# Optimization experiments

Hardware: AMD Instinct MI355X
Metric: run time of the kernel (lower is better)

The kernel has to match this reference:

```python
import jax, jax.numpy as jnp
import numpy as np

B = 131072
EPS = 1e-5

def _attn(x, Wq, Wk, Wv, Wo):
    # x: (B, 10, 1); Wq/Wk/Wv: (1, 16); Wo: (16, 1)
    Q = x @ Wq  # (B, 10, 16)
    K = x @ Wk
    V = x @ Wv
    A = jnp.einsum('bqd,bkd->bqk', Q, K) / 4.0  # sqrt(16) = 4
    A = jax.nn.softmax(A, axis=1)  # NOTE: torch Softmax(dim=1) -> axis 1, not -1
    out = jnp.einsum('bqk,bkd->bqd', A, V) @ Wo  # (B, 10, 1)
    return out[..., 0]  # squeeze -> (B, 10)

def _bn(h, gamma, beta):
    # BatchNorm1d training-mode math (batch stats, biased variance)
    mu = jnp.mean(h, axis=0)
    var = jnp.mean(jnp.square(h - mu), axis=0)
    return gamma * (h - mu) * jax.lax.rsqrt(var + EPS) + beta

def setup_inputs() -> dict:
    key = jax.random.key(0)
    ks = jax.random.split(key, 24)
    n = lambda k, shp, s=1.0: (jax.random.normal(k, shp, dtype=jnp.float32) * s)
    inp = {
        'x':   n(ks[0], (B, 10, 1)),
        'Wq1': n(ks[1], (1, 16)), 'Wk1': n(ks[2], (1, 16)),
        'Wv1': n(ks[3], (1, 16)), 'Wo1': n(ks[4], (16, 1)),
        'Wq2': n(ks[5], (1, 16)), 'Wk2': n(ks[6], (1, 16)),
        'Wv2': n(ks[7], (1, 16)), 'Wo2': n(ks[8], (16, 1)),
        # layer1: Linear(10,128) BN ReLU Linear(128,256) BN ReLU Linear(256,10)
        'W1a': n(ks[9], (10, 128), 0.3), 'b1a': jnp.zeros((128,), jnp.float32),
        'g1a': jnp.ones((128,), jnp.float32), 'be1a': jnp.zeros((128,), jnp.float32),
        'W1b': n(ks[10], (128, 256), 0.09), 'b1b': jnp.zeros((256,), jnp.float32),
        'g1b': jnp.ones((256,), jnp.float32), 'be1b': jnp.zeros((256,), jnp.float32),
        'W1c': n(ks[11], (256, 10), 0.06), 'b1c': jnp.zeros((10,), jnp.float32),
        # layer2: Linear(10,128) BN ReLU Linear(128,256) BN ReLU Linear(256,2)
        'W2a': n(ks[12], (10, 128), 0.3), 'b2a': jnp.zeros((128,), jnp.float32),
        'g2a': jnp.ones((128,), jnp.float32), 'be2a': jnp.zeros((128,), jnp.float32),
        'W2b': n(ks[13], (128, 256), 0.09), 'b2b': jnp.zeros((256,), jnp.float32),
        'g2b': jnp.ones((256,), jnp.float32), 'be2b': jnp.zeros((256,), jnp.float32),
        'W2c': n(ks[14], (256, 2), 0.06), 'b2c': jnp.zeros((2,), jnp.float32),
    }
    return inp

def reference(x, Wq1, Wk1, Wv1, Wo1, Wq2, Wk2, Wv2, Wo2,
              W1a, b1a, g1a, be1a, W1b, b1b, g1b, be1b, W1c, b1c,
              W2a, b2a, g2a, be2a, W2b, b2b, g2b, be2b, W2c, b2c):
    h = _attn(x, Wq1, Wk1, Wv1, Wo1)                 # (B, 10)
    h = jax.nn.relu(_bn(h @ W1a + b1a, g1a, be1a))   # (B, 128)
    h = jax.nn.relu(_bn(h @ W1b + b1b, g1b, be1b))   # (B, 256)
    h = h @ W1c + b1c                                # (B, 10)
    h = _attn(h[..., None], Wq2, Wk2, Wv2, Wo2)      # (B, 10)
    h = jax.nn.relu(_bn(h @ W2a + b2a, g2a, be2a))   # (B, 128)
    h = jax.nn.relu(_bn(h @ W2b + b2b, g2b, be2b))   # (B, 256)
    return h @ W2c + b2c                             # (B, 2)
```

## Files before the change

kernel.cpp:

```cpp
#include <hip/hip_runtime.h>
#include <hip/hip_bf16.h>

#define EPS 1e-5f
constexpr int BN = 131072;
constexpr int NBKT = 32;
constexpr int NTILE = BN/64;
constexpr int TILE_ELEMS = 256*64;

typedef __attribute__((ext_vector_type(8))) short bf16x8;
typedef __attribute__((ext_vector_type(4))) float f32x4;

constexpr size_t OFF_H   = 0;
constexpr size_t OFF_HH  = OFF_H  + (size_t)BN*10;
constexpr size_t OFF_M1  = OFF_HH + (size_t)BN*10;
constexpr size_t OFF_S2  = OFF_M1 + 65;
constexpr size_t OFF_M3  = OFF_S2 + 512;
constexpr size_t OFF_S4  = OFF_M3 + 65;
constexpr size_t OFF_WA1 = OFF_S4 + 512;
constexpr size_t OFF_BA1 = OFF_WA1 + 1280;
constexpr size_t OFF_WA2 = OFF_BA1 + 128;
constexpr size_t OFF_BA2 = OFF_WA2 + 1280;
constexpr size_t OFF_SC2 = OFF_BA2 + 128;
constexpr size_t OFF_TC2 = OFF_SC2 + 256;
constexpr size_t OFF_SC4 = OFF_TC2 + 256;
constexpr size_t OFF_TC4 = OFF_SC4 + 256;
constexpr size_t OFF_WB1 = OFF_TC4 + 256;
constexpr size_t OFF_BB1 = OFF_WB1 + 32768;
constexpr size_t OFF_WB2 = OFF_BB1 + 256;
constexpr size_t OFF_BB2 = OFF_WB2 + 32768;
constexpr size_t OFF_P1  = OFF_BB2 + 256;
constexpr size_t OFF_P3  = OFF_P1 + 1024*65;
constexpr size_t OFF_S2B = OFF_P3 + 1024*65;
constexpr size_t OFF_S4B = OFF_S2B + (size_t)NBKT*512;
constexpr size_t OFF_WT1 = OFF_S4B + (size_t)NBKT*512;
constexpr size_t OFF_WT2 = OFF_WT1 + 16384;
constexpr size_t OFF_END = OFF_WT2 + 16384;
constexpr size_t OFF_Z_BYTES = ((OFF_END*4 + 255) & ~(size_t)255);
constexpr size_t WS_NEED = OFF_Z_BYTES + (size_t)NTILE*TILE_ELEMS*2;

__device__ __forceinline__ float wsum(float v){
  v += __shfl_down(v, 32);
  v += __shfl_down(v, 16);
  v += __shfl_down(v, 8);
  v += __shfl_down(v, 4);
  v += __shfl_down(v, 2);
  v += __shfl_down(v, 1);
  return v;
}

__device__ __forceinline__ unsigned pk_bf16(float a, float b){
  union { __hip_bfloat16 h[2]; unsigned u; } cv;
  cv.h[0] = __float2bfloat16(a);
  cv.h[1] = __float2bfloat16(b);
  return cv.u;
}

__device__ __forceinline__ unsigned short bf16_1(float a){
  union { __hip_bfloat16 h; unsigned short u; } cv;
  cv.h = __float2bfloat16(a);
  return cv.u;
}

__device__ __forceinline__ float bf16_to_f(unsigned short u){
  return __uint_as_float(((unsigned)u) << 16);
}

__device__ __forceinline__ void attn10(const float* xr, float cqk, float cvo, float* y){
  #pragma unroll
  for (int q=0;q<10;q++) y[q] = 0.f;
  #pragma unroll
  for (int k=0;k<10;k++){
    float t = cqk * xr[k];
    float m = t*xr[0];
    #pragma unroll
    for (int q=1;q<10;q++) m = fmaxf(m, t*xr[q]);
    float ex[10]; float s = 0.f;
    #pragma unroll
    for (int q=0;q<10;q++){ ex[q] = __expf(t*xr[q]-m); s += ex[q]; }
    float f = xr[k]/s;
    #pragma unroll
    for (int q=0;q<10;q++) y[q] += ex[q]*f;
  }
  #pragma unroll
  for (int q=0;q<10;q++) y[q] *= cvo;
}

__device__ __forceinline__ void moments_block(const float* y, float (*red)[65],
                                              float* Pb, int t){
  int lane = t & 63, w = t >> 6;
  #pragma unroll
  for (int i=0;i<10;i++){
    float v = wsum(y[i]);
    if (lane==0) red[w][i] = v;
  }
  #pragma unroll
  for (int i=0;i<10;i++){
    #pragma unroll
    for (int j=i;j<10;j++){
      float v = wsum(y[i]*y[j]);
      if (lane==0) red[w][10 + 10*i - i*(i-1)/2 + (j-i)] = v;
    }
  }
  __syncthreads();
  if (t < 65)
    Pb[(size_t)blockIdx.x*65 + t] = red[0][t]+red[1][t]+red[2][t]+red[3][t];
}

__device__ __forceinline__ void moments10(const float* y, float* M, int lane){
  #pragma unroll
  for (int i=0;i<10;i++){
    float s = wsum(y[i]);
    if (lane==0) atomicAdd(&M[i], s);
  }
  #pragma unroll
  for (int i=0;i<10;i++){
    #pragma unroll
    for (int j=i;j<10;j++){
      int id = 10*i - i*(i-1)/2 + (j-i);
      float s = wsum(y[i]*y[j]);
      if (lane==0) atomicAdd(&M[10+id], s);
    }
  }
}

__global__ __launch_bounds__(256) void k_attn_in(
    const float* __restrict__ x,
    const float* __restrict__ Wq, const float* __restrict__ Wk,
    const float* __restrict__ Wv, const float* __restrict__ Wo,
    float* __restrict__ h, float* __restrict__ Pb){
  __shared__ float xs[256][11];
  __shared__ float red[4][65];
  int t = threadIdx.x;
  size_t base = (size_t)blockIdx.x*2560;
  for (int idx=t; idx<2560; idx+=256) xs[idx/10][idx%10] = x[base+idx];
  float cqk=0.f, cvo=0.f;
  #pragma unroll
  for (int d=0;d<16;d++){ cqk += Wq[d]*Wk[d]; cvo += Wv[d]*Wo[d]; }
  cqk *= 0.25f;
  __syncthreads();
  float xr[10];
  #pragma unroll
  for (int q=0;q<10;q++) xr[q] = xs[t][q];
  float y[10];
  attn10(xr, cqk, cvo, y);
  #pragma unroll
  for (int q=0;q<10;q++) xs[t][q] = y[q];
  moments_block(y, red, Pb, t);
  for (int idx=t; idx<2560; idx+=256) h[base+idx] = xs[idx/10][idx%10];
}

__global__ void k_fold10_part(const float* __restrict__ Pb, int npart,
                              const float* __restrict__ W,
                              const float* __restrict__ bv, const float* __restrict__ g,
                              const float* __restrict__ be,
                              float* __restrict__ WT, float* __restrict__ bo){
  __shared__ float part[65][8];
  __shared__ float sM[65];
  int t = threadIdx.x;
  if (t < 520){
    int c = t>>3, k = t&7;
    int n = npart>>3;
    float acc = 0.f;
    #pragma unroll 4
    for (int i=0;i<n;i++) acc += Pb[(size_t)(k*n+i)*65 + c];
    part[c][k] = acc;
  }
  __syncthreads();
  if (t < 65){
    float a = 0.f;
    #pragma unroll
    for (int k=0;k<8;k++) a += part[t][k];
    sM[t] = a;
  }
  __syncthreads();
  int j = t;
  if (j >= 128) return;
  const float invB = 1.f/(float)BN;
  float Eh[10];
  #pragma unroll
  for (int i=0;i<10;i++) Eh[i] = sM[i]*invB;
  float wj[10];
  #pragma unroll
  for (int i=0;i<10;i++) wj[i] = W[i*128+j];
  float mu = bv[j];
  #pragma unroll
  for (int i=0;i<10;i++) mu += Eh[i]*wj[i];
  float var = 0.f;
  #pragma unroll
  for (int i=0;i<10;i++){
    #pragma unroll
    for (int l=0;l<10;l++){
      int a = i<l ? i : l, c = i<l ? l : i;
      int id = 10*a - a*(a-1)/2 + (c-a);
      float cov = sM[10+id]*invB - Eh[i]*Eh[l];
      var += wj[i]*wj[l]*cov;
    }
  }
  float s = g[j]*rsqrtf(var + EPS);
  #pragma unroll
  for (int i=0;i<10;i++) WT[j*10+i] = wj[i]*s;
  bo[j] = (bv[j]-mu)*s + be[j];
}

__global__ void k_fold10_atomic(const float* __restrict__ M,
                                const float* __restrict__ W,
                                const float* __restrict__ bv, const float* __restrict__ g,
                                const float* __restrict__ be,
                                float* __restrict__ WT, float* __restrict__ bo){
  int j = threadIdx.x;
  if (j >= 128) return;
  const float invB = 1.f/(float)BN;
  float Eh[10];
  #pragma unroll
  for (int i=0;i<10;i++) Eh[i] = M[i]*invB;
  float wj[10];
  #pragma unroll
  for (int i=0;i<10;i++) wj[i] = W[i*128+j];
  float mu = bv[j];
  #pragma unroll
  for (int i=0;i<10;i++) mu += Eh[i]*wj[i];
  float var = 0.f;
  #pragma unroll
  for (int i=0;i<10;i++){
    #pragma unroll
    for (int l=0;l<10;l++){
      int a = i<l ? i : l, c = i<l ? l : i;
      int id = 10*a - a*(a-1)/2 + (c-a);
      float cov = M[10+id]*invB - Eh[i]*Eh[l];
      var += wj[i]*wj[l]*cov;
    }
  }
  float s = g[j]*rsqrtf(var + EPS);
  #pragma unroll
  for (int i=0;i<10;i++) WT[j*10+i] = wj[i]*s;
  bo[j] = (bv[j]-mu)*s + be[j];
}

__global__ void k_fold_affine(const float* __restrict__ stats,
                              const float* __restrict__ g,
                              const float* __restrict__ be,
                              float* __restrict__ s, float* __restrict__ tt){
  int j = threadIdx.x;
  if (j >= 256) return;
  float su = 0.f, sq = 0.f;
  #pragma unroll 4
  for (int k=0;k<NBKT;k++){
    su += stats[k*512 + j];
    sq += stats[k*512 + 256 + j];
  }
  const float invB = 1.f/(float)BN;
  float mu  = su*invB;
  float var = sq*invB - mu*mu;
  float sc = g[j]*rsqrtf(var + EPS);
  s[j]  = sc;
  tt[j] = be[j] - mu*sc;
}

__global__ __launch_bounds__(256) void k_prep_wt2(
    const float* __restrict__ W1, const float* __restrict__ W2,
    unsigned short* __restrict__ WT1, unsigned short* __restrict__ WT2){
  int g = blockIdx.x;
  const float* W = (g < 128) ? W1 : W2;
  unsigned short* WT = (g < 128) ? WT1 : WT2;
  int idx = (g & 127)*256 + threadIdx.x;
  int c = idx >> 7, k = idx & 127;
  WT[idx] = bf16_1(W[k*256 + c]);
}

__device__ __forceinline__ void block_gemm(
    const float* __restrict__ h, const float* __restrict__ WaT,
    const float* __restrict__ ba, const unsigned short* __restrict__ WT,
    unsigned short* h1s, float (*hs)[11], float* sWaT,
    f32x4 (&acc)[4][4], int t, size_t row0)
{
  int lane = t & 63, w = t >> 6;
  int ci = lane & 15, g = lane >> 4;

  bf16x8 bfr[4][4];
  #pragma unroll
  for (int nt=0; nt<4; nt++)
    #pragma unroll
    for (int kt=0; kt<4; kt++){
      union { uint4 u; bf16x8 v; } cv;
      cv.u = *(const uint4*)(WT + (size_t)(w*64 + nt*16 + ci)*128 + kt*32 + g*8);
      bfr[nt][kt] = cv.v;
    }

  for (int idx = t; idx < 640; idx += 256) hs[idx/10][idx%10] = h[row0*10 + idx];
  for (int idx = t; idx < 1280; idx += 256) sWaT[idx] = WaT[idx];
  __syncthreads();

  {
    int r = lane;
    int i0 = w * 32;
    float hr[10];
    #pragma unroll
    for (int l=0;l<10;l++) hr[l] = hs[r][l];
    #pragma unroll
    for (int j=0;j<4;j++){
      unsigned pk[4];
      #pragma unroll
      for (int q=0;q<4;q++){
        int i = i0 + j*8 + q*2;
        float v0 = ba[i], v1 = ba[i+1];
        #pragma unroll
        for (int l=0;l<10;l++){
          v0 = fmaf(hr[l], sWaT[i*10+l],     v0);
          v1 = fmaf(hr[l], sWaT[(i+1)*10+l], v1);
        }
        pk[q] = pk_bf16(fmaxf(v0,0.f), fmaxf(v1,0.f));
      }
      int byte = r*256 + (((i0 + j*8)*2) ^ ((r&7)<<4));
      *(uint4*)((char*)h1s + byte) = make_uint4(pk[0],pk[1],pk[2],pk[3]);
    }
  }
  __syncthreads();

  #pragma unroll
  for (int mt=0;mt<4;mt++)
    #pragma unroll
    for (int nt=0;nt<4;nt++)
      acc[mt][nt] = (f32x4){0.f,0.f,0.f,0.f};

  #pragma unroll
  for (int mt=0; mt<4; mt++){
    int r = mt*16 + ci;
    bf16x8 af[4];
    #pragma unroll
    for (int kt=0; kt<4; kt++){
      int byte = r*256 + ((kt*64 + g*16) ^ ((r&7)<<4));
      af[kt] = *(const bf16x8*)((const char*)h1s + byte);
    }
    #pragma unroll
    for (int nt=0; nt<4; nt++)
      #pragma unroll
      for (int kt=0; kt<4; kt++)
        acc[mt][nt] = __builtin_amdgcn_mfma_f32_16x16x32_bf16(
            af[kt], bfr[nt][kt], acc[mt][nt], 0, 0, 0);
  }
}

__global__ __launch_bounds__(256) void k_layer_mfma(
    const float* __restrict__ h,
    const float* __restrict__ WaT,
    const float* __restrict__ ba,
    const unsigned short* __restrict__ WT,
    const float* __restrict__ bb,
    unsigned short* __restrict__ zt,
    float* __restrict__ stats)
{
  __shared__ __align__(16) char smem[36864];
  unsigned short* h1s = (unsigned short*)smem;
  float (*hs)[11]     = (float(*)[11])(smem + 16384);
  float* sWaT         = (float*)(smem + 19200);
  unsigned short* zs  = (unsigned short*)smem;
  int t = threadIdx.x;
  int lane = t & 63, w = t >> 6;
  int ci = lane & 15, g = lane >> 4;
  size_t row0 = (size_t)blockIdx.x * 64;

  f32x4 acc[4][4];
  block_gemm(h, WaT, ba, WT, h1s, hs, sWaT, acc, t, row0);

  float bbv[4];
  #pragma unroll
  for (int nt=0;nt<4;nt++) bbv[nt] = bb[w*64 + nt*16 + ci];
  float s1v[4], s2v[4];
  #pragma unroll
  for (int nt=0; nt<4; nt++){
    float cs = 0.f, cq = 0.f;
    #pragma unroll
    for (int mt=0; mt<4; mt++)
      #pragma unroll
      for (int j=0;j<4;j++){
        float zv = acc[mt][nt][j] + bbv[nt];
        acc[mt][nt][j] = zv;
        cs += zv;
        cq += zv*zv;
      }
    cs += __shfl_down(cs, 32); cs += __shfl_down(cs, 16);
    cq += __shfl_down(cq, 32); cq += __shfl_down(cq, 16);
    s1v[nt] = cs; s2v[nt] = cq;
  }
  __syncthreads();

  #pragma unroll
  for (int mt=0; mt<4; mt++)
    #pragma unroll
    for (int nt=0; nt<4; nt++){
      int c = w*64 + nt*16 + ci;
      int r0 = mt*16 + g*4;
      uint2 v;
      v.x = pk_bf16(acc[mt][nt][0], acc[mt][nt][1]);
      v.y = pk_bf16(acc[mt][nt][2], acc[mt][nt][3]);
      *(uint2*)&zs[c*72 + r0] = v;
    }
  __syncthreads();

  size_t tbase = (size_t)blockIdx.x * TILE_ELEMS;
  #pragma unroll
  for (int pass=0; pass<8; pass++){
    int c  = (t>>3) + pass*32;
    int rc = (t&7)*8;
    uint4 v = *(const uint4*)&zs[c*72 + rc];
    *(uint4*)(zt + tbase + c*64 + rc) = v;
  }

  if (lane < 16){
    int bkt = blockIdx.x & (NBKT-1);
    #pragma unroll
    for (int nt=0; nt<4; nt++){
      int c = w*64 + nt*16 + ci;
      atomicAdd(&stats[bkt*512 + c],       s1v[nt]);
      atomicAdd(&stats[bkt*512 + 256 + c], s2v[nt]);
    }
  }
}

__global__ __launch_bounds__(256) void k_consume_mid(
    const unsigned short* __restrict__ zt,
    const float* __restrict__ s_g, const float* __restrict__ t_g,
    const float* __restrict__ Wc,  const float* __restrict__ bc,
    const float* __restrict__ Wq, const float* __restrict__ Wk,
    const float* __restrict__ Wv, const float* __restrict__ Wo,
    float* __restrict__ hh, float* __restrict__ Pb){
  __shared__ __align__(16) unsigned short zs[2][32*256];
  __shared__ __align__(16) float sWc[256*12];
  __shared__ float ss[256], st[256];
  __shared__ float red[4][65];
  int t = threadIdx.x;
  for (int idx=t; idx<2560; idx+=256) sWc[(idx/10)*12 + (idx%10)] = Wc[idx];
  ss[t] = s_g[t]; st[t] = t_g[t];
  size_t b0 = (size_t)blockIdx.x*256;

  float z3[10];
  #pragma unroll
  for (int l=0;l<10;l++) z3[l] = bc[l];

  int q = t >> 6, l = t & 63;
  size_t src_base = ((size_t)blockIdx.x*4 + q)*TILE_ELEMS + l*32;
  int dst_off = (l>>1)*256 + q*64 + (l&1)*32;
  uint4 r0, r1, r2, r3;
  {
    const uint4* src = (const uint4*)(zt + src_base);
    r0 = src[0]; r1 = src[1]; r2 = src[2]; r3 = src[3];
    uint4* dst = (uint4*)&zs[0][dst_off];
    dst[0] = r0; dst[1] = r1; dst[2] = r2; dst[3] = r3;
  }
  for (int cc=0; cc<8; cc++){
    __syncthreads();
    if (cc < 7){
      const uint4* src = (const uint4*)(zt + src_base + (size_t)(cc+1)*2048);
      r0 = src[0]; r1 = src[1]; r2 = src[2]; r3 = src[3];
    }
    const unsigned short* zb = zs[cc&1];
    #pragma unroll 4
    for (int cl=0; cl<32; cl++){
      int c = cc*32 + cl;
      float f = bf16_to_f(zb[cl*256 + t]);
      float h2 = fmaxf(fmaf(ss[c], f, st[c]), 0.f);
      const float4* wr = (const float4*)&sWc[c*12];
      float4 w0 = wr[0];
      float4 w1 = wr[1];
      float2 w2 = *(const float2*)&sWc[c*12 + 8];
      z3[0] = fmaf(h2, w0.x, z3[0]); z3[1] = fmaf(h2, w0.y, z3[1]);
      z3[2] = fmaf(h2, w0.z, z3[2]); z3[3] = fmaf(h2, w0.w, z3[3]);
      z3[4] = fmaf(h2, w1.x, z3[4]); z3[5] = fmaf(h2, w1.y, z3[5]);
      z3[6] = fmaf(h2, w1.z, z3[6]); z3[7] = fmaf(h2, w1.w, z3[7]);
      z3[8] = fmaf(h2, w2.x, z3[8]); z3[9] = fmaf(h2, w2.y, z3[9]);
    }
    if (cc < 7){
      uint4* dst = (uint4*)&zs[(cc+1)&1][dst_off];
      dst[0] = r0; dst[1] = r1; dst[2] = r2; dst[3] = r3;
    }
  }

  float cqk=0.f, cvo=0.f;
  #pragma unroll
  for (int d=0;d<16;d++){ cqk += Wq[d]*Wk[d]; cvo += Wv[d]*Wo[d]; }
  cqk *= 0.25f;
  float y[10];
  attn10(z3, cqk, cvo, y);
  __syncthreads();
  float* hhs = (float*)zs[0];
  #pragma unroll
  for (int qq=0;qq<10;qq++) hhs[t*10+qq] = y[qq];
  moments_block(y, red, Pb, t);
  for (int idx=t; idx<2560; idx+=256)
    hh[b0*10 + idx] = hhs[idx];
}

__global__ __launch_bounds__(256) void k_consume_out(
    const unsigned short* __restrict__ zt,
    const float* __restrict__ s_g, const float* __restrict__ t_g,
    const float* __restrict__ Wc,  const float* __restrict__ bc,
    float* __restrict__ out){
  __shared__ __align__(16) unsigned short zs[2][32*256];
  __shared__ __align__(8) float sWo[512];
  __shared__ float ss[256], st[256];
  int t = threadIdx.x;
  sWo[t] = Wc[t]; sWo[256+t] = Wc[256+t];
  ss[t] = s_g[t]; st[t] = t_g[t];
  size_t b0 = (size_t)blockIdx.x*256;
  float o0 = bc[0], o1 = bc[1];
  int q = t >> 6, l = t & 63;
  size_t src_base = ((size_t)blockIdx.x*4 + q)*TILE_ELEMS + l*32;
  int dst_off = (l>>1)*256 + q*64 + (l&1)*32;
  uint4 r0, r1, r2, r3;
  {
    const uint4* src = (const uint4*)(zt + src_base);
    r0 = src[0]; r1 = src[1]; r2 = src[2]; r3 = src[3];
    uint4* dst = (uint4*)&zs[0][dst_off];
    dst[0] = r0; dst[1] = r1; dst[2] = r2; dst[3] = r3;
  }
  for (int cc=0; cc<8; cc++){
    __syncthreads();
    if (cc < 7){
      const uint4* src = (const uint4*)(zt + src_base + (size_t)(cc+1)*2048);
      r0 = src[0]; r1 = src[1]; r2 = src[2]; r3 = src[3];
    }
    const unsigned short* zb = zs[cc&1];
    #pragma unroll 8
    for (int cl=0; cl<32; cl++){
      int c = cc*32 + cl;
      float f = bf16_to_f(zb[cl*256 + t]);
      float h5 = fmaxf(fmaf(ss[c], f, st[c]), 0.f);
      float2 wv = *(const float2*)&sWo[c*2];
      o0 = fmaf(h5, wv.x, o0);
      o1 = fmaf(h5, wv.y, o1);
    }
    if (cc < 7){
      uint4* dst = (uint4*)&zs[(cc+1)&1][dst_off];
      dst[0] = r0; dst[1] = r1; dst[2] = r2; dst[3] = r3;
    }
  }
  *(float2*)(out + (b0 + t)*2) = make_float2(o0, o1);
}

__global__ void k_fold_big(const float* __restrict__ stats,
                           const float* __restrict__ W,
                           const float* __restrict__ bv, const float* __restrict__ g,
                           const float* __restrict__ be,
                           float* __restrict__ Wf, float* __restrict__ bf){
  int j = blockIdx.x*256 + threadIdx.x;
  if (j >= 256) return;
  const float invB = 1.f/(float)BN;
  float mu  = stats[j]*invB;
  float var = stats[256+j]*invB - mu*mu;
  float s = g[j]*rsqrtf(var + EPS);
  bf[j] = (bv[j]-mu)*s + be[j];
  for (int i=0;i<128;i++) Wf[i*256+j] = W[i*256+j]*s;
}

__global__ __launch_bounds__(256) void k_mid(
    const float* __restrict__ h,
    const float* __restrict__ WaT, const float* __restrict__ ba,
    const float* __restrict__ Wb,  const float* __restrict__ bb,
    float* __restrict__ stats){
  int b = blockIdx.x*256 + threadIdx.x;
  if (b >= BN) return;
  float hr[10];
  #pragma unroll
  for (int l=0;l<10;l++) hr[l] = h[(size_t)b*10+l];
  int lane = threadIdx.x & 63;
  for (int jc=0;jc<4;jc++){
    float acc[64];
    #pragma unroll
    for (int j=0;j<64;j++) acc[j] = bb[jc*64+j];
    for (int i=0;i<128;i++){
      float h1 = ba[i];
      #pragma unroll
      for (int l=0;l<10;l++) h1 += hr[l]*WaT[i*10+l];
      h1 = fmaxf(h1, 0.f);
      const float* __restrict__ w = &Wb[i*256 + jc*64];
      #pragma unroll
      for (int j=0;j<64;j++) acc[j] += h1*w[j];
    }
    #pragma unroll
    for (int j=0;j<64;j++){
      float s1 = wsum(acc[j]);
      float s2 = wsum(acc[j]*acc[j]);
      if (lane==0){
        atomicAdd(&stats[jc*64+j], s1);
        atomicAdd(&stats[256+jc*64+j], s2);
      }
    }
  }
}

__global__ __launch_bounds__(256) void k_mid2(
    const float* __restrict__ h,
    const float* __restrict__ WaT, const float* __restrict__ ba,
    const float* __restrict__ Wbf, const float* __restrict__ bbf,
    const float* __restrict__ Wc,  const float* __restrict__ bc,
    const float* __restrict__ Wq, const float* __restrict__ Wk,
    const float* __restrict__ Wv, const float* __restrict__ Wo,
    float* __restrict__ hh, float* __restrict__ M){
  int b = blockIdx.x*256 + threadIdx.x;
  if (b >= BN) return;
  float hr[10];
  #pragma unroll
  for (int l=0;l<10;l++) hr[l] = h[(size_t)b*10+l];
  float z3[10];
  #pragma unroll
  for (int l=0;l<10;l++) z3[l] = bc[l];
  for (int jc=0;jc<4;jc++){
    float acc[64];
    #pragma unroll
    for (int j=0;j<64;j++) acc[j] = bbf[jc*64+j];
    for (int i=0;i<128;i++){
      float h1 = ba[i];
      #pragma unroll
      for (int l=0;l<10;l++) h1 += hr[l]*WaT[i*10+l];
      h1 = fmaxf(h1, 0.f);
      const float* __restrict__ w = &Wbf[i*256 + jc*64];
      #pragma unroll
      for (int j=0;j<64;j++) acc[j] += h1*w[j];
    }
    #pragma unroll
    for (int j=0;j<64;j++){
      float h2 = fmaxf(acc[j], 0.f);
      const float* __restrict__ wc = &Wc[(jc*64+j)*10];
      #pragma unroll
      for (int l=0;l<10;l++) z3[l] += h2*wc[l];
    }
  }
  float cqk=0.f, cvo=0.f;
  #pragma unroll
  for (int d=0;d<16;d++){ cqk += Wq[d]*Wk[d]; cvo += Wv[d]*Wo[d]; }
  cqk *= 0.25f;
  float y[10];
  attn10(z3, cqk, cvo, y);
  #pragma unroll
  for (int q=0;q<10;q++) hh[(size_t)b*10+q] = y[q];
  moments10(y, M, threadIdx.x & 63);
}

__global__ __launch_bounds__(256) void k_out(
    const float* __restrict__ h,
    const float* __restrict__ WaT, const float* __restrict__ ba,
    const float* __restrict__ Wbf, const float* __restrict__ bbf,
    const float* __restrict__ Wc,  const float* __restrict__ bc,
    float* __restrict__ out){
  int b = blockIdx.x*256 + threadIdx.x;
  if (b >= BN) return;
  float hr[10];
  #pragma unroll
  for (int l=0;l<10;l++) hr[l] = h[(size_t)b*10+l];
  float o0 = bc[0], o1 = bc[1];
  for (int jc=0;jc<4;jc++){
    float acc[64];
    #pragma unroll
    for (int j=0;j<64;j++) acc[j] = bbf[jc*64+j];
    for (int i=0;i<128;i++){
      float h4 = ba[i];
      #pragma unroll
      for (int l=0;l<10;l++) h4 += hr[l]*WaT[i*10+l];
      h4 = fmaxf(h4, 0.f);
      const float* __restrict__ w = &Wbf[i*256 + jc*64];
      #pragma unroll
      for (int j=0;j<64;j++) acc[j] += h4*w[j];
    }
    #pragma unroll
    for (int j=0;j<64;j++){
      float h5 = fmaxf(acc[j], 0.f);
      o0 += h5*Wc[(jc*64+j)*2];
      o1 += h5*Wc[(jc*64+j)*2+1];
    }
  }
  out[(size_t)b*2]   = o0;
  out[(size_t)b*2+1] = o1;
}

extern "C" void kernel_launch(void* const* d_in, const int* in_sizes, int n_in,
                              void* d_out, int out_size, void* d_ws, size_t ws_size,
                              hipStream_t stream){
  const float* x   = (const float*)d_in[0];
  const float* Wq1 = (const float*)d_in[1];
  const float* Wk1 = (const float*)d_in[2];
  const float* Wv1 = (const float*)d_in[3];
  const float* Wo1 = (const float*)d_in[4];
  const float* Wq2 = (const float*)d_in[5];
  const float* Wk2 = (const float*)d_in[6];
  const float* Wv2 = (const float*)d_in[7];
  const float* Wo2 = (const float*)d_in[8];
  const float* W1a = (const float*)d_in[9];  const float* b1a = (const float*)d_in[10];
  const float* g1a = (const float*)d_in[11]; const float* be1a= (const float*)d_in[12];
  const float* W1b = (const float*)d_in[13]; const float* b1b = (const float*)d_in[14];
  const float* g1b = (const float*)d_in[15]; const float* be1b= (const float*)d_in[16];
  const float* W1c = (const float*)d_in[17]; const float* b1c = (const float*)d_in[18];
  const float* W2a = (const float*)d_in[19]; const float* b2a = (const float*)d_in[20];
  const float* g2a = (const float*)d_in[21]; const float* be2a= (const float*)d_in[22];
  const float* W2b = (const float*)d_in[23]; const float* b2b = (const float*)d_in[24];
  const float* g2b = (const float*)d_in[25]; const float* be2b= (const float*)d_in[26];
  const float* W2c = (const float*)d_in[27]; const float* b2c = (const float*)d_in[28];

  float* f   = (float*)d_ws;
  float* h   = f + OFF_H;
  float* hh  = f + OFF_HH;
  float* M1  = f + OFF_M1;
  float* S2  = f + OFF_S2;
  float* M3  = f + OFF_M3;
  float* S4  = f + OFF_S4;
  float* WA1 = f + OFF_WA1; float* BA1 = f + OFF_BA1;
  float* WA2 = f + OFF_WA2; float* BA2 = f + OFF_BA2;
  float* SC2 = f + OFF_SC2; float* TC2 = f + OFF_TC2;
  float* SC4 = f + OFF_SC4; float* TC4 = f + OFF_TC4;
  float* WB1 = f + OFF_WB1; float* BB1 = f + OFF_BB1;
  float* WB2 = f + OFF_WB2; float* BB2 = f + OFF_BB2;
  float* P1  = f + OFF_P1;  float* P3  = f + OFF_P3;
  float* S2B = f + OFF_S2B; float* S4B = f + OFF_S4B;
  unsigned short* WT1 = (unsigned short*)(f + OFF_WT1);
  unsigned short* WT2 = (unsigned short*)(f + OFF_WT2);
  unsigned short* ZT = (unsigned short*)((char*)d_ws + OFF_Z_BYTES);

  dim3 blk(256);
  dim3 grid256(BN/256);
  dim3 grid64(BN/64);

  if (ws_size >= WS_NEED){
    hipMemsetAsync(S2B, 0, (size_t)2*NBKT*512*sizeof(float), stream);
    k_prep_wt2<<<256,blk,0,stream>>>(W1b, W2b, WT1, WT2);
    k_attn_in<<<grid256,blk,0,stream>>>(x, Wq1,Wk1,Wv1,Wo1, h, P1);
    k_fold10_part<<<1,576,0,stream>>>(P1, 512, W1a,b1a,g1a,be1a, WA1,BA1);
    k_layer_mfma<<<grid64,blk,0,stream>>>(h, WA1,BA1, WT1,b1b, ZT, S2B);
    k_fold_affine<<<1,256,0,stream>>>(S2B, g1b, be1b, SC2, TC2);
    k_consume_mid<<<grid256,blk,0,stream>>>(ZT, SC2,TC2, W1c,b1c,
                                            Wq2,Wk2,Wv2,Wo2, hh, P3);
    k_fold10_part<<<1,576,0,stream>>>(P3, 512, W2a,b2a,g2a,be2a, WA2,BA2);
    k_layer_mfma<<<grid64,blk,0,stream>>>(hh, WA2,BA2, WT2,b2b, ZT, S4B);
    k_fold_affine<<<1,256,0,stream>>>(S4B, g2b, be2b, SC4, TC4);
    k_consume_out<<<grid256,blk,0,stream>>>(ZT, SC4,TC4, W2c,b2c, (float*)d_out);
  } else {
    hipMemsetAsync(M1, 0, (65+512+65+512)*sizeof(float), stream);
    k_attn_in<<<grid256,blk,0,stream>>>(x, Wq1,Wk1,Wv1,Wo1, h, P1);
    k_fold10_part<<<1,576,0,stream>>>(P1, 512, W1a,b1a,g1a,be1a, WA1,BA1);
    k_mid<<<grid256,blk,0,stream>>>(h, WA1,BA1, W1b,b1b, S2);
    k_fold_big<<<1,256,0,stream>>>(S2, W1b,b1b,g1b,be1b, WB1,BB1);
    k_mid2<<<grid256,blk,0,stream>>>(h, WA1,BA1, WB1,BB1, W1c,b1c,
                                     Wq2,Wk2,Wv2,Wo2, hh, M3);
    k_fold10_atomic<<<1,128,0,stream>>>(M3, W2a,b2a,g2a,be2a, WA2,BA2);
    k_mid<<<grid256,blk,0,stream>>>(hh, WA2,BA2, W2b,b2b, S4);
    k_fold_big<<<1,256,0,stream>>>(S4, W2b,b2b,g2b,be2b, WB2,BB2);
    k_out<<<grid256,blk,0,stream>>>(hh, WA2,BA2, WB2,BB2, W2c,b2c, (float*)d_out);
  }
}
```

Baseline: 214.9 us.

## Process two 64-row tiles per block and store GEMM output directly

k_layer_mfma now handles 128 rows per block as two 64-row tiles. The bf16 weight fragments held in registers are reused across both tiles, halving their global loads and the number of atomic stat flushes per row. The LDS transpose staging of the output is dropped: each lane writes its packed 8-byte values straight to the tiled global buffer, and the second tile's layer-a compute goes into a separate LDS buffer. The direct stores are narrower and less coalesced than the old 16-byte ones, and halving the grid reduces block-level parallelism.

```diff
diff --git a/kernel.cpp b/kernel.cpp
--- a/kernel.cpp
+++ b/kernel.cpp
@@ -267,14 +267,22 @@
   WT[idx] = bf16_1(W[k*256 + c]);
 }
 
-__device__ __forceinline__ void block_gemm(
-    const float* __restrict__ h, const float* __restrict__ WaT,
-    const float* __restrict__ ba, const unsigned short* __restrict__ WT,
-    unsigned short* h1s, float (*hs)[11], float* sWaT,
-    f32x4 (&acc)[4][4], int t, size_t row0)
+__global__ __launch_bounds__(256) void k_layer_mfma(
+    const float* __restrict__ h,
+    const float* __restrict__ WaT,
+    const float* __restrict__ ba,
+    const unsigned short* __restrict__ WT,
+    const float* __restrict__ bb,
+    unsigned short* __restrict__ zt,
+    float* __restrict__ stats)
 {
+  __shared__ unsigned short h1s[2][64*128];
+  __shared__ float hs[128][11];
+  __shared__ float sWaT[1280];
+  int t = threadIdx.x;
   int lane = t & 63, w = t >> 6;
   int ci = lane & 15, g = lane >> 4;
+  size_t row0 = (size_t)blockIdx.x * 128;
 
   bf16x8 bfr[4][4];
   #pragma unroll
@@ -286,9 +294,14 @@
       bfr[nt][kt] = cv.v;
     }
 
-  for (int idx = t; idx < 640; idx += 256) hs[idx/10][idx%10] = h[row0*10 + idx];
+  for (int idx = t; idx < 1280; idx += 256) hs[idx/10][idx%10] = h[row0*10 + idx];
   for (int idx = t; idx < 1280; idx += 256) sWaT[idx] = WaT[idx];
   __syncthreads();
+
+  float bbv[4];
+  #pragma unroll
+  for (int nt=0;nt<4;nt++) bbv[nt] = bb[w*64 + nt*16 + ci];
+  float cs[4] = {0,0,0,0}, cq[4] = {0,0,0,0};
 
   {
     int r = lane;
@@ -311,17 +324,17 @@
         pk[q] = pk_bf16(fmaxf(v0,0.f), fmaxf(v1,0.f));
       }
       int byte = r*256 + (((i0 + j*8)*2) ^ ((r&7)<<4));
-      *(uint4*)((char*)h1s + byte) = make_uint4(pk[0],pk[1],pk[2],pk[3]);
+      *(uint4*)((char*)h1s[0] + byte) = make_uint4(pk[0],pk[1],pk[2],pk[3]);
     }
   }
   __syncthreads();
 
+  f32x4 acc[4][4];
   #pragma unroll
   for (int mt=0;mt<4;mt++)
     #pragma unroll
     for (int nt=0;nt<4;nt++)
       acc[mt][nt] = (f32x4){0.f,0.f,0.f,0.f};
-
   #pragma unroll
   for (int mt=0; mt<4; mt++){
     int r = mt*16 + ci;
@@ -329,7 +342,7 @@
     #pragma unroll
     for (int kt=0; kt<4; kt++){
       int byte = r*256 + ((kt*64 + g*16) ^ ((r&7)<<4));
-      af[kt] = *(const bf16x8*)((const char*)h1s + byte);
+      af[kt] = *(const bf16x8*)((const char*)h1s[0] + byte);
     }
     #pragma unroll
     for (int nt=0; nt<4; nt++)
@@ -338,81 +351,103 @@
         acc[mt][nt] = __builtin_amdgcn_mfma_f32_16x16x32_bf16(
             af[kt], bfr[nt][kt], acc[mt][nt], 0, 0, 0);
   }
-}
-
-__global__ __launch_bounds__(256) void k_layer_mfma(
-    const float* __restrict__ h,
-    const float* __restrict__ WaT,
-    const float* __restrict__ ba,
-    const unsigned short* __restrict__ WT,
-    const float* __restrict__ bb,
-    unsigned short* __restrict__ zt,
-    float* __restrict__ stats)
-{
-  __shared__ __align__(16) char smem[36864];
-  unsigned short* h1s = (unsigned short*)smem;
-  float (*hs)[11]     = (float(*)[11])(smem + 16384);
-  float* sWaT         = (float*)(smem + 19200);
-  unsigned short* zs  = (unsigned short*)smem;
-  int t = threadIdx.x;
-  int lane = t & 63, w = t >> 6;
-  int ci = lane & 15, g = lane >> 4;
-  size_t row0 = (size_t)blockIdx.x * 64;
-
-  f32x4 acc[4][4];
-  block_gemm(h, WaT, ba, WT, h1s, hs, sWaT, acc, t, row0);
-
-  float bbv[4];
-  #pragma unroll
-  for (int nt=0;nt<4;nt++) bbv[nt] = bb[w*64 + nt*16 + ci];
-  float s1v[4], s2v[4];
-  #pragma unroll
-  for (int nt=0; nt<4; nt++){
-    float cs = 0.f, cq = 0.f;
-    #pragma unroll
-    for (int mt=0; mt<4; mt++)
-      #pragma unroll
-      for (int j=0;j<4;j++){
-        float zv = acc[mt][nt][j] + bbv[nt];
-        acc[mt][nt][j] = zv;
-        cs += zv;
-        cq += zv*zv;
-      }
-    cs += __shfl_down(cs, 32); cs += __shfl_down(cs, 16);
-    cq += __shfl_down(cq, 32); cq += __shfl_down(cq, 16);
-    s1v[nt] = cs; s2v[nt] = cq;
-  }
-  __syncthreads();
-
-  #pragma unroll
-  for (int mt=0; mt<4; mt++)
+
+  {
+    size_t tbase = ((size_t)blockIdx.x*2 + 0) * TILE_ELEMS;
     #pragma unroll
     for (int nt=0; nt<4; nt++){
       int c = w*64 + nt*16 + ci;
-      int r0 = mt*16 + g*4;
-      uint2 v;
-      v.x = pk_bf16(acc[mt][nt][0], acc[mt][nt][1]);
-      v.y = pk_bf16(acc[mt][nt][2], acc[mt][nt][3]);
-      *(uint2*)&zs[c*72 + r0] = v;
-    }
+      #pragma unroll
+      for (int mt=0; mt<4; mt++){
+        float z0 = acc[mt][nt][0] + bbv[nt];
+        float z1 = acc[mt][nt][1] + bbv[nt];
+        float z2 = acc[mt][nt][2] + bbv[nt];
+        float z3 = acc[mt][nt][3] + bbv[nt];
+        cs[nt] += z0+z1+z2+z3;
+        cq[nt] += z0*z0+z1*z1+z2*z2+z3*z3;
+        *(uint2*)(zt + tbase + c*64 + mt*16 + g*4) =
+            make_uint2(pk_bf16(z0,z1), pk_bf16(z2,z3));
+      }
+    }
+  }
+
+  {
+    int r = lane;
+    int i0 = w * 32;
+    float hr[10];
+    #pragma unroll
+    for (int l=0;l<10;l++) hr[l] = hs[64 + r][l];
+    #pragma unroll
+    for (int j=0;j<4;j++){
+      unsigned pk[4];
+      #pragma unroll
+      for (int q=0;q<4;q++){
+        int i = i0 + j*8 + q*2;
+        float v0 = ba[i], v1 = ba[i+1];
+        #pragma unroll
+        for (int l=0;l<10;l++){
+          v0 = fmaf(hr[l], sWaT[i*10+l],     v0);
+          v1 = fmaf(hr[l], sWaT[(i+1)*10+l], v1);
+        }
+        pk[q] = pk_bf16(fmaxf(v0,0.f), fmaxf(v1,0.f));
+      }
+      int byte = r*256 + (((i0 + j*8)*2) ^ ((r&7)<<4));
+      *(uint4*)((char*)h1s[1] + byte) = make_uint4(pk[0],pk[1],pk[2],pk[3]);
+    }
+  }
   __syncthreads();
 
-  size_t tbase = (size_t)blockIdx.x * TILE_ELEMS;
-  #pragma unroll
-  for (int pass=0; pass<8; pass++){
-    int c  = (t>>3) + pass*32;
-    int rc = (t&7)*8;
-    uint4 v = *(const uint4*)&zs[c*72 + rc];
-    *(uint4*)(zt + tbase + c*64 + rc) = v;
-  }
-
-  if (lane < 16){
-    int bkt = blockIdx.x & (NBKT-1);
+  #pragma unroll
+  for (int mt=0;mt<4;mt++)
+    #pragma unroll
+    for (int nt=0;nt<4;nt++)
+      acc[mt][nt] = (f32x4){0.f,0.f,0.f,0.f};
+  #pragma unroll
+  for (int mt=0; mt<4; mt++){
+    int r = mt*16 + ci;
+    bf16x8 af[4];
+    #pragma unroll
+    for (int kt=0; kt<4; kt++){
+      int byte = r*256 + ((kt*64 + g*16) ^ ((r&7)<<4));
+      af[kt] = *(const bf16x8*)((const char*)h1s[1] + byte);
+    }
+    #pragma unroll
+    for (int nt=0; nt<4; nt++)
+      #pragma unroll
+      for (int kt=0; kt<4; kt++)
+        acc[mt][nt] = __builtin_amdgcn_mfma_f32_16x16x32_bf16(
+            af[kt], bfr[nt][kt], acc[mt][nt], 0, 0, 0);
+  }
+
+  {
+    size_t tbase = ((size_t)blockIdx.x*2 + 1) * TILE_ELEMS;
     #pragma unroll
     for (int nt=0; nt<4; nt++){
       int c = w*64 + nt*16 + ci;
-      atomicAdd(&stats[bkt*512 + c],       s1v[nt]);
-      atomicAdd(&stats[bkt*512 + 256 + c], s2v[nt]);
+      #pragma unroll
+      for (int mt=0; mt<4; mt++){
+        float z0 = acc[mt][nt][0] + bbv[nt];
+        float z1 = acc[mt][nt][1] + bbv[nt];
+        float z2 = acc[mt][nt][2] + bbv[nt];
+        float z3 = acc[mt][nt][3] + bbv[nt];
+        cs[nt] += z0+z1+z2+z3;
+        cq[nt] += z0*z0+z1*z1+z2*z2+z3*z3;
+        *(uint2*)(zt + tbase + c*64 + mt*16 + g*4) =
+            make_uint2(pk_bf16(z0,z1), pk_bf16(z2,z3));
+      }
+    }
+  }
+
+  #pragma unroll
+  for (int nt=0; nt<4; nt++){
+    float s1 = cs[nt], s2 = cq[nt];
+    s1 += __shfl_down(s1, 32); s1 += __shfl_down(s1, 16);
+    s2 += __shfl_down(s2, 32); s2 += __shfl_down(s2, 16);
+    if (lane < 16){
+      int bkt = blockIdx.x & (NBKT-1);
+      int c = w*64 + nt*16 + ci;
+      atomicAdd(&stats[bkt*512 + c],       s1);
+      atomicAdd(&stats[bkt*512 + 256 + c], s2);
     }
   }
 }
@@ -716,19 +751,19 @@
 
   dim3 blk(256);
   dim3 grid256(BN/256);
-  dim3 grid64(BN/64);
+  dim3 grid128(BN/128);
 
   if (ws_size >= WS_NEED){
     hipMemsetAsync(S2B, 0, (size_t)2*NBKT*512*sizeof(float), stream);
     k_prep_wt2<<<256,blk,0,stream>>>(W1b, W2b, WT1, WT2);
     k_attn_in<<<grid256,blk,0,stream>>>(x, Wq1,Wk1,Wv1,Wo1, h, P1);
     k_fold10_part<<<1,576,0,stream>>>(P1, 512, W1a,b1a,g1a,be1a, WA1,BA1);
-    k_layer_mfma<<<grid64,blk,0,stream>>>(h, WA1,BA1, WT1,b1b, ZT, S2B);
+    k_layer_mfma<<<grid128,blk,0,stream>>>(h, WA1,BA1, WT1,b1b, ZT, S2B);
     k_fold_affine<<<1,256,0,stream>>>(S2B, g1b, be1b, SC2, TC2);
     k_consume_mid<<<grid256,blk,0,stream>>>(ZT, SC2,TC2, W1c,b1c,
                                             Wq2,Wk2,Wv2,Wo2, hh, P3);
     k_fold10_part<<<1,576,0,stream>>>(P3, 512, W2a,b2a,g2a,be2a, WA2,BA2);
-    k_layer_mfma<<<grid64,blk,0,stream>>>(hh, WA2,BA2, WT2,b2b, ZT, S4B);
+    k_layer_mfma<<<grid128,blk,0,stream>>>(hh, WA2,BA2, WT2,b2b, ZT, S4B);
     k_fold_affine<<<1,256,0,stream>>>(S4B, g2b, be2b, SC4, TC4);
     k_consume_out<<<grid256,blk,0,stream>>>(ZT, SC4,TC4, W2c,b2c, (float*)d_out);
   } else {
```

Result: faster. 207.8 us (median of 3 runs) (-3.3%).
